# Optimization experiments

Hardware: AMD Instinct MI355X
Metric: run time of the kernel (lower is better)

## Reference

```python
import jax, jax.numpy as jnp
import numpy as np

TOPK = 4
ROUTE_SCALE = 1.0


def setup_inputs() -> dict:
    key = jax.random.key(0)
    ks = jax.random.split(key, 16)
    B, S, C, D = 4, 512, 4, 2048
    E, H = 16, 1408
    SH = 2 * H  # n_shared_experts * moe_inter_dim
    s = 0.02
    return {
        "embeddings": jax.random.normal(ks[0], (B, S, C, D), jnp.float32),
        "x": jax.random.normal(ks[1], (B, S, C, 1), jnp.float32),
        "Wg": jax.random.normal(ks[2], (E, D), jnp.float32) * s,
        "W1": jax.random.normal(ks[3], (E, H, D), jnp.float32) * s,
        "b1": jax.random.normal(ks[4], (E, H), jnp.float32) * s,
        "W2": jax.random.normal(ks[5], (E, D, H), jnp.float32) * s,
        "b2": jax.random.normal(ks[6], (E, D), jnp.float32) * s,
        "W3": jax.random.normal(ks[7], (E, H, D), jnp.float32) * s,
        "b3": jax.random.normal(ks[8], (E, H), jnp.float32) * s,
        "Ws1": jax.random.normal(ks[9], (SH, D), jnp.float32) * s,
        "bs1": jax.random.normal(ks[10], (SH,), jnp.float32) * s,
        "Ws2": jax.random.normal(ks[11], (D, SH), jnp.float32) * s,
        "bs2": jax.random.normal(ks[12], (D,), jnp.float32) * s,
    }


def reference(embeddings, x, Wg, W1, b1, W2, b2, W3, b3, Ws1, bs1, Ws2, bs2):
    # NOTE: in the torch module, the `x` arg is immediately shadowed by
    # embeddings.view(-1, dim); it does not participate in the math.
    D = Wg.shape[1]
    E = Wg.shape[0]
    xt = embeddings.reshape(-1, D)  # [N, D] flattened tokens

    # Gate: softmax scores (fp32), top-k routing; n_groups == 1, no gate bias.
    logits = jnp.einsum("nd,ed->ne", xt, Wg)
    scores = jax.nn.softmax(logits.astype(jnp.float32), axis=-1)  # [N, E]
    topv, idx = jax.lax.top_k(scores, TOPK)  # values == gathered original scores
    weights = (topv * ROUTE_SCALE).astype(xt.dtype)  # [N, K]

    # Expert dispatch/combine. Per-token combined weight for expert e is
    # sum_k weights[n, k] * (idx[n, k] == e); unassigned tokens get weight 0,
    # so masked-dense per-expert SwiGLU reproduces the gather/scatter math.
    y = jnp.zeros_like(xt)
    for e in range(E):
        w_e = jnp.sum(weights * (idx == e).astype(weights.dtype), axis=1)  # [N]
        h = jax.nn.silu(xt @ W1[e].T + b1[e]) * (xt @ W3[e].T + b3[e])  # [N, H]
        y = y + (h @ W2[e].T + b2[e]) * w_e[:, None]

    # Shared experts: Linear -> SiLU -> Linear applied to every token.
    z = jax.nn.silu(xt @ Ws1.T + bs1) @ Ws2.T + bs2

    return (y + z).reshape(embeddings.shape)
```

## Files before the change

### kernel.cpp

```cpp
#include <hip/hip_runtime.h>
#include <stdint.h>

#define N_TOK 8192
#define DIM   2048
#define NEXP  16
#define HID   1408
#define SHID  2816
#define KTOP  4
#define TILEMAX 272

typedef __attribute__((ext_vector_type(8))) short bf16x8;
typedef __attribute__((ext_vector_type(4))) float f32x4;

#define MFMA16(a,b,c) __builtin_amdgcn_mfma_f32_16x16x32_bf16((a),(b),(c),0,0,0)

__device__ __forceinline__ unsigned short f2b(float f){
  unsigned u = __float_as_uint(f);
  return (unsigned short)((u + 0x7fffu + ((u >> 16) & 1u)) >> 16);
}
__device__ __forceinline__ unsigned pk2(float a, float b){
  return (unsigned)f2b(a) | ((unsigned)f2b(b) << 16);
}
__device__ __forceinline__ float bu2f(unsigned hs){ return __uint_as_float(hs << 16); }
__device__ __forceinline__ float siluf(float x){ return x / (1.f + expf(-x)); }
__device__ __forceinline__ f32x4 zero4(){ f32x4 z; z[0]=0.f; z[1]=0.f; z[2]=0.f; z[3]=0.f; return z; }

__device__ __forceinline__ void gll16(const unsigned short* g, unsigned short* l){
  __builtin_amdgcn_global_load_lds(
      (const __attribute__((address_space(1))) void*)g,
      (__attribute__((address_space(3))) void*)l, 16, 0, 0);
}

#define SEGW ((size_t)NEXP*HID*DIM/4)
#define SEGS ((size_t)SHID*DIM/4)
__global__ __launch_bounds__(256) void k_cvtW(const float* __restrict__ W1, const float* __restrict__ W3,
                                              const float* __restrict__ W2, const float* __restrict__ Ws1,
                                              const float* __restrict__ Ws2,
                                              unsigned short* __restrict__ d1, unsigned short* __restrict__ d3,
                                              unsigned short* __restrict__ d2, unsigned short* __restrict__ ds1,
                                              unsigned short* __restrict__ ds2){
  size_t total = 3*SEGW + 2*SEGS;
  for (size_t i = (size_t)blockIdx.x*256 + threadIdx.x; i < total; i += (size_t)gridDim.x*256){
    const float* s; unsigned short* d; size_t off;
    if      (i <   SEGW)        { s = W1;  d = d1;  off = i; }
    else if (i < 2*SEGW)        { s = W3;  d = d3;  off = i - SEGW; }
    else if (i < 3*SEGW)        { s = W2;  d = d2;  off = i - 2*SEGW; }
    else if (i < 3*SEGW + SEGS) { s = Ws1; d = ds1; off = i - 3*SEGW; }
    else                        { s = Ws2; d = ds2; off = i - 3*SEGW - SEGS; }
    float4 v = ((const float4*)s)[off];
    uint2 q; q.x = pk2(v.x, v.y); q.y = pk2(v.z, v.w);
    ((uint2*)d)[off] = q;
  }
}

__global__ __launch_bounds__(256) void k_gate(const float* __restrict__ X, const float* __restrict__ Wg,
                                              float* __restrict__ topw, int* __restrict__ topi,
                                              int* __restrict__ cnt, unsigned short* __restrict__ Xb){
  int lane = threadIdx.x & 63;
  int t = blockIdx.x*4 + (threadIdx.x >> 6);
  const float* xr = X + (size_t)t*DIM;
  float4 xv[8];
#pragma unroll
  for (int i=0;i<8;i++){
    xv[i] = *(const float4*)(xr + i*256 + lane*4);
    uint2 q; q.x = pk2(xv[i].x, xv[i].y); q.y = pk2(xv[i].z, xv[i].w);
    *(uint2*)(Xb + (size_t)t*DIM + i*256 + lane*4) = q;
  }
  float sc[NEXP];
#pragma unroll
  for (int e=0;e<NEXP;e++){
    const float* wr = Wg + e*DIM;
    float s = 0.f;
#pragma unroll
    for (int i=0;i<8;i++){
      float4 w = *(const float4*)(wr + i*256 + lane*4);
      s = fmaf(xv[i].x, w.x, s); s = fmaf(xv[i].y, w.y, s);
      s = fmaf(xv[i].z, w.z, s); s = fmaf(xv[i].w, w.w, s);
    }
#pragma unroll
    for (int d=1; d<64; d<<=1) s += __shfl_xor(s, d);
    sc[e] = s;
  }
  if (lane == 0){
    float m = sc[0];
#pragma unroll
    for (int e=1;e<NEXP;e++) m = fmaxf(m, sc[e]);
    float den = 0.f;
#pragma unroll
    for (int e=0;e<NEXP;e++){ sc[e] = expf(sc[e]-m); den += sc[e]; }
    float inv = 1.f/den;
#pragma unroll
    for (int e=0;e<NEXP;e++) sc[e] *= inv;
    for (int k=0;k<KTOP;k++){
      int bi = 0; float bv = sc[0];
#pragma unroll
      for (int e=1;e<NEXP;e++) if (sc[e] > bv){ bv = sc[e]; bi = e; }
      topw[t*KTOP+k] = bv;
      topi[t*KTOP+k] = bi;
#pragma unroll
      for (int e=0;e<NEXP;e++) if (e == bi) sc[e] = -1.f;
      atomicAdd(&cnt[bi], 1);
    }
  }
}

__global__ void k_scan(const int* __restrict__ cnt, int* __restrict__ off, int* __restrict__ cur,
                       int* __restrict__ tab){
  if (threadIdx.x == 0){
    int a = 0;
    for (int e=0;e<NEXP;e++){ off[e] = a; cur[e] = a; a += cnt[e]; }
    int n = 0;
    for (int e=0;e<NEXP;e++){
      int nt = (cnt[e] + 127) >> 7;
      for (int r=0;r<nt;r++) tab[n++] = (e << 16) | r;
    }
    for (; n < TILEMAX; ++n) tab[n] = -1;
  }
}

__global__ __launch_bounds__(256) void k_place(const int* __restrict__ topi, const float* __restrict__ topw,
                                               int* __restrict__ cur, int* __restrict__ rows,
                                               float* __restrict__ rw, int* __restrict__ slotL){
  int t = blockIdx.x*256 + threadIdx.x;
#pragma unroll
  for (int k=0;k<KTOP;k++){
    int e = topi[t*KTOP+k];
    int p = atomicAdd(&cur[e], 1);
    rows[p] = t;
    rw[p]   = topw[t*KTOP+k];
    slotL[t*KTOP+k] = p;
  }
}

__device__ __forceinline__ void stage_Bf(unsigned short* lsB, const float* bF,
                                         int ldK, int bn0, int k0, int tid){
#pragma unroll
  for (int j=0;j<8;j++){
    int idx = j*256 + tid, r = idx >> 4, c4 = idx & 15;
    float4 v = *(const float4*)(bF + (size_t)(bn0 + r)*ldK + k0 + c4*4);
    uint2 q; q.x = pk2(v.x, v.y); q.y = pk2(v.z, v.w);
    *(uint2*)&lsB[r*64 + (((c4 >> 1) ^ (r & 7)) << 3) + ((c4 & 1) << 2)] = q;
  }
}

__device__ __forceinline__ void read_A(bf16x8 af[4], const unsigned short* lsA, int wm, int lane, int kc){
  int s = kc*4 + (lane >> 4);
#pragma unroll
  for (int mi=0;mi<4;mi++){
    int r = wm + mi*16 + (lane & 15);
    af[mi] = *(const bf16x8*)&lsA[r*64 + ((s ^ (r & 7)) << 3)];
  }
}

template<bool WBF>
__global__ __launch_bounds__(256,2) void k_g13(const unsigned short* __restrict__ Xb,
    const void* __restrict__ W1p, const void* __restrict__ W3p,
    const float* __restrict__ b1, const float* __restrict__ b3,
    const int* __restrict__ rows, const int* __restrict__ cnt, const int* __restrict__ offs,
    const int* __restrict__ tab, unsigned short* __restrict__ H1)
{
  int bid = blockIdx.x;
  int l = bid >> 3;
  int ct = l / 34;
  int slot = (bid & 7)*34 + (l - ct*34);
  int ent = tab[slot];
  if (ent < 0) return;
  int e = ent >> 16, rt = ent & 0xffff;
  int cntE = cnt[e];
  int offE = offs[e];
  int hn0 = ct*128;
  int tid = threadIdx.x, lane = tid & 63, wid = tid >> 6;
  int wm = (wid >> 1)*64, wn = (wid & 1)*64;
  __shared__ alignas(16) unsigned short lsA[8192], lsB1[8192], lsB3[8192];

  int lr8 = lane >> 3;
  int cx  = (lane & 7) ^ lr8;
  unsigned offA[4];
#pragma unroll
  for (int j=0;j<4;j++){
    int lrow = rt*128 + wid*32 + j*8 + lr8;
    int arow = rows[offE + (lrow < cntE ? lrow : cntE-1)];
    offA[j] = (unsigned)arow*DIM + (unsigned)cx*8;
  }
  unsigned offB0 = (unsigned)(hn0 + wid*32 + lr8)*DIM + (unsigned)cx*8;
  const unsigned short* b1H = (const unsigned short*)W1p + (size_t)e*HID*DIM;
  const unsigned short* b3H = (const unsigned short*)W3p + (size_t)e*HID*DIM;
  const float* b1F = (const float*)W1p + (size_t)e*HID*DIM;
  const float* b3F = (const float*)W3p + (size_t)e*HID*DIM;
  unsigned short* lA  = &lsA[wid*2048];
  unsigned short* lB1 = &lsB1[wid*2048];
  unsigned short* lB3 = &lsB3[wid*2048];

  f32x4 acc1[4][4], acc3[4][4];
#pragma unroll
  for (int i=0;i<4;i++)
#pragma unroll
    for (int j=0;j<4;j++){ acc1[i][j] = zero4(); acc3[i][j] = zero4(); }

  for (int kt=0; kt<DIM/64; ++kt){
    int k0 = kt*64;
    __syncthreads();
#pragma unroll
    for (int j=0;j<4;j++){
      gll16(Xb + offA[j] + k0, lA + j*512);
      if constexpr (WBF){
        gll16(b1H + offB0 + j*(8*DIM) + k0, lB1 + j*512);
        gll16(b3H + offB0 + j*(8*DIM) + k0, lB3 + j*512);
      }
    }
    if constexpr (!WBF){
      stage_Bf(lsB1, b1F, DIM, hn0, k0, tid);
      stage_Bf(lsB3, b3F, DIM, hn0, k0, tid);
    }
    __syncthreads();
#pragma unroll
    for (int kc=0;kc<2;kc++){
      bf16x8 af[4]; read_A(af, lsA, wm, lane, kc);
      int sB = kc*4 + (lane >> 4);
#pragma unroll
      for (int nj=0;nj<4;nj++){
        int rb = wn + nj*16 + (lane & 15);
        int lof = rb*64 + ((sB ^ (rb & 7)) << 3);
        bf16x8 bf1 = *(const bf16x8*)&lsB1[lof];
        bf16x8 bf3 = *(const bf16x8*)&lsB3[lof];
#pragma unroll
        for (int mi=0;mi<4;mi++){
          acc1[mi][nj] = MFMA16(af[mi], bf1, acc1[mi][nj]);
          acc3[mi][nj] = MFMA16(af[mi], bf3, acc3[mi][nj]);
        }
      }
    }
  }
#pragma unroll
  for (int nj=0;nj<4;nj++){
    int h = hn0 + wn + nj*16 + (lane & 15);
    float b1v = b1[e*HID + h];
    float b3v = b3[e*HID + h];
#pragma unroll
    for (int mi=0;mi<4;mi++){
#pragma unroll
      for (int r=0;r<4;r++){
        int gr = rt*128 + wm + mi*16 + (lane >> 4)*4 + r;
        if (gr < cntE){
          float u = acc1[mi][nj][r] + b1v;
          float v = acc3[mi][nj][r] + b3v;
          H1[(size_t)(offE + gr)*HID + h] = f2b(siluf(u)*v);
        }
      }
    }
  }
}

template<int MODE, bool WBF, int KSTEPS>
__global__ __launch_bounds__(256,2) void k_gemm(const unsigned short* __restrict__ Abase,
    const void* __restrict__ Bpv, const float* __restrict__ bias,
    float* __restrict__ outF, unsigned short* __restrict__ outH,
    const int* __restrict__ rows, const float* __restrict__ rw,
    const int* __restrict__ cnt, const int* __restrict__ offs,
    const int* __restrict__ tab)
{
  constexpr bool EXPERT = (MODE == 2 || MODE == 3);
  constexpr int KD = KSTEPS*64;
  int e = 0, ct, rt, cntE = 0, offE = 0;
  int bid = blockIdx.x;
  int l = bid >> 3;
  if constexpr (EXPERT){
    ct = l / 34;
    int slot = (bid & 7)*34 + (l - ct*34);
    int ent = tab[slot];
    if (ent < 0) return;
    e = ent >> 16; rt = ent & 0xffff;
    cntE = cnt[e];
    offE = offs[e];
  } else {
    rt = (bid & 7)*8 + (l & 7);
    ct = l >> 3;
  }
  int bn0 = ct*128, t0 = rt*128;
  int tid = threadIdx.x, lane = tid & 63, wid = tid >> 6;
  int wm = (wid >> 1)*64, wn = (wid & 1)*64;
  __shared__ alignas(16) unsigned short lsA[8192], lsB[8192];

  int lr8 = lane >> 3;
  int cx  = (lane & 7) ^ lr8;
  unsigned offA0 = 0;
  unsigned offA[4];
  if constexpr (EXPERT){
#pragma unroll
    for (int j=0;j<4;j++){
      int lrow = t0 + wid*32 + j*8 + lr8;
      int arow = offE + (lrow < cntE ? lrow : cntE-1);
      offA[j] = (unsigned)arow*KD + (unsigned)cx*8;
    }
  } else {
    offA0 = (unsigned)(t0 + wid*32 + lr8)*KD + (unsigned)cx*8;
  }
  unsigned offB0 = (unsigned)(bn0 + wid*32 + lr8)*KD + (unsigned)cx*8;
  const unsigned short* bH = (const unsigned short*)Bpv + (EXPERT ? (size_t)e*2048*KD : (size_t)0);
  const float*          bF = (const float*)Bpv          + (EXPERT ? (size_t)e*2048*KD : (size_t)0);
  const float* biasp = bias + (EXPERT ? e*DIM : 0);
  unsigned short* lA = &lsA[wid*2048];
  unsigned short* lB = &lsB[wid*2048];

  f32x4 acc[4][4];
#pragma unroll
  for (int i=0;i<4;i++)
#pragma unroll
    for (int j=0;j<4;j++) acc[i][j] = zero4();

  for (int kt=0; kt<KSTEPS; ++kt){
    int k0 = kt*64;
    __syncthreads();
#pragma unroll
    for (int j=0;j<4;j++){
      if constexpr (EXPERT) gll16(Abase + offA[j] + k0, lA + j*512);
      else                  gll16(Abase + offA0 + j*(8*KD) + k0, lA + j*512);
      if constexpr (WBF)    gll16(bH + offB0 + j*(8*KD) + k0, lB + j*512);
    }
    if constexpr (!WBF) stage_Bf(lsB, bF, KD, bn0, k0, tid);
    __syncthreads();
#pragma unroll
    for (int kc=0;kc<2;kc++){
      bf16x8 af[4]; read_A(af, lsA, wm, lane, kc);
      int sB = kc*4 + (lane >> 4);
#pragma unroll
      for (int nj=0;nj<4;nj++){
        int rb = wn + nj*16 + (lane & 15);
        bf16x8 bfr = *(const bf16x8*)&lsB[rb*64 + ((sB ^ (rb & 7)) << 3)];
#pragma unroll
        for (int mi=0;mi<4;mi++)
          acc[mi][nj] = MFMA16(af[mi], bfr, acc[mi][nj]);
      }
    }
  }
#pragma unroll
  for (int nj=0;nj<4;nj++){
    int col = bn0 + wn + nj*16 + (lane & 15);
    float bv = biasp[col];
#pragma unroll
    for (int mi=0;mi<4;mi++){
#pragma unroll
      for (int r=0;r<4;r++){
        int lr = wm + mi*16 + (lane >> 4)*4 + r;
        float v = acc[mi][nj][r] + bv;
        if constexpr (MODE == 0){
          outH[(size_t)(t0 + lr)*SHID + col] = f2b(siluf(v));
        } else if constexpr (MODE == 1){
          outF[(size_t)(t0 + lr)*DIM + col] = v;
        } else {
          int gr = t0 + lr;
          if (gr < cntE){
            int slot = offE + gr;
            float wv = rw[slot] * v;
            if constexpr (MODE == 2){
              atomicAdd(outF + (size_t)rows[slot]*DIM + col, wv);
            } else {
              outH[(size_t)slot*DIM + col] = f2b(wv);
            }
          }
        }
      }
    }
  }
}

__global__ __launch_bounds__(256) void k_comb(const unsigned short* __restrict__ Yr,
                                              const int* __restrict__ slotL, float* __restrict__ out){
  int i = blockIdx.x*256 + threadIdx.x;
  int t = i >> 8, c = i & 255;
  size_t ob = (size_t)t*DIM + (size_t)c*8;
  float4 a = *(float4*)(out + ob);
  float4 b = *(float4*)(out + ob + 4);
  int sl[4];
#pragma unroll
  for (int k=0;k<KTOP;k++) sl[k] = slotL[t*KTOP + k];
#pragma unroll
  for (int k=0;k<KTOP;k++){
    uint4 v = *(const uint4*)(Yr + (size_t)sl[k]*DIM + (size_t)c*8);
    a.x += bu2f(v.x & 0xffffu); a.y += bu2f(v.x >> 16);
    a.z += bu2f(v.y & 0xffffu); a.w += bu2f(v.y >> 16);
    b.x += bu2f(v.z & 0xffffu); b.y += bu2f(v.z >> 16);
    b.z += bu2f(v.w & 0xffffu); b.w += bu2f(v.w >> 16);
  }
  *(float4*)(out + ob) = a;
  *(float4*)(out + ob + 4) = b;
}

extern "C" void kernel_launch(void* const* d_in, const int* in_sizes, int n_in,
                              void* d_out, int out_size, void* d_ws, size_t ws_size,
                              hipStream_t stream)
{
  (void)in_sizes; (void)n_in; (void)out_size;
  const float* emb = (const float*)d_in[0];
  const float* Wg  = (const float*)d_in[2];
  const float* W1  = (const float*)d_in[3];
  const float* b1  = (const float*)d_in[4];
  const float* W2  = (const float*)d_in[5];
  const float* b2  = (const float*)d_in[6];
  const float* W3  = (const float*)d_in[7];
  const float* b3  = (const float*)d_in[8];
  const float* Ws1 = (const float*)d_in[9];
  const float* bs1 = (const float*)d_in[10];
  const float* Ws2 = (const float*)d_in[11];
  const float* bs2 = (const float*)d_in[12];
  float* out = (float*)d_out;
  char* ws = (char*)d_ws;

  const size_t SZ_XB = (size_t)N_TOK*DIM*2;
  const size_t SZ_H1 = (size_t)N_TOK*KTOP*HID*2;
  const size_t SZ_HS = (size_t)N_TOK*SHID*2;
  const size_t SZ_T4 = (size_t)N_TOK*KTOP*4;
  const size_t SZ_WB = (size_t)NEXP*HID*DIM*2;
  const size_t SZ_SB = (size_t)SHID*DIM*2;
  const size_t SZ_YR = (size_t)N_TOK*KTOP*DIM*2;

  size_t off_xb = 0;
  size_t off_h1 = off_xb + SZ_XB;
  size_t off_hs = off_h1 + SZ_H1;
  size_t off_tw = off_hs + SZ_HS;
  size_t off_ti = off_tw + SZ_T4;
  size_t off_ro = off_ti + SZ_T4;
  size_t off_rw = off_ro + SZ_T4;
  size_t off_sl = off_rw + SZ_T4;
  size_t off_cnt = off_sl + SZ_T4;
  size_t off_off = off_cnt + 256;
  size_t off_cur = off_off + 256;
  size_t off_tab = off_cur + 256;
  size_t base_end = off_tab + TILEMAX*4 + 64;
  size_t off_w1b = base_end;
  size_t off_w3b = off_w1b + SZ_WB;
  size_t off_w2b = off_w3b + SZ_WB;
  size_t off_s1b = off_w2b + SZ_WB;
  size_t off_s2b = off_s1b + SZ_SB;
  size_t wbf_end = off_s2b + SZ_SB;

  bool wbf = ws_size >= wbf_end;
  size_t off_yr = wbf ? wbf_end : base_end;
  bool comb = ws_size >= off_yr + SZ_YR;

  unsigned short* Xb = (unsigned short*)(ws + off_xb);
  unsigned short* H1 = (unsigned short*)(ws + off_h1);
  unsigned short* Hs = (unsigned short*)(ws + off_hs);
  float* topw = (float*)(ws + off_tw);
  int*   topi = (int*)(ws + off_ti);
  int*   rowsL= (int*)(ws + off_ro);
  float* rwL  = (float*)(ws + off_rw);
  int*   slotL= (int*)(ws + off_sl);
  int*   cntP = (int*)(ws + off_cnt);
  int*   offP = (int*)(ws + off_off);
  int*   curP = (int*)(ws + off_cur);
  int*   tabP = (int*)(ws + off_tab);
  unsigned short* Yr = (unsigned short*)(ws + off_yr);

  hipMemsetAsync(ws + off_cnt, 0, 768, stream);
  if (wbf){
    k_cvtW<<<4096, 256, 0, stream>>>(W1, W3, W2, Ws1, Ws2,
        (unsigned short*)(ws + off_w1b), (unsigned short*)(ws + off_w3b),
        (unsigned short*)(ws + off_w2b), (unsigned short*)(ws + off_s1b),
        (unsigned short*)(ws + off_s2b));
  }
  k_gate<<<2048, 256, 0, stream>>>(emb, Wg, topw, topi, cntP, Xb);
  k_scan<<<1, 64, 0, stream>>>(cntP, offP, curP, tabP);
  k_place<<<32, 256, 0, stream>>>(topi, topw, curP, rowsL, rwL, slotL);

  if (wbf) k_g13<true ><<<2992, 256, 0, stream>>>(Xb, ws+off_w1b, ws+off_w3b, b1, b3, rowsL, cntP, offP, tabP, H1);
  else     k_g13<false><<<2992, 256, 0, stream>>>(Xb, W1, W3, b1, b3, rowsL, cntP, offP, tabP, H1);

  if (wbf) k_gemm<0,true ,32><<<1408, 256, 0, stream>>>(Xb, ws+off_s1b, bs1, nullptr, Hs, nullptr,nullptr,nullptr,nullptr,nullptr);
  else     k_gemm<0,false,32><<<1408, 256, 0, stream>>>(Xb, Ws1, bs1, nullptr, Hs, nullptr,nullptr,nullptr,nullptr,nullptr);

  if (wbf) k_gemm<1,true ,44><<<1024, 256, 0, stream>>>(Hs, ws+off_s2b, bs2, out, nullptr, nullptr,nullptr,nullptr,nullptr,nullptr);
  else     k_gemm<1,false,44><<<1024, 256, 0, stream>>>(Hs, Ws2, bs2, out, nullptr, nullptr,nullptr,nullptr,nullptr,nullptr);

  if (comb){
    if (wbf) k_gemm<3,true ,22><<<4352, 256, 0, stream>>>(H1, ws+off_w2b, b2, nullptr, Yr, rowsL, rwL, cntP, offP, tabP);
    else     k_gemm<3,false,22><<<4352, 256, 0, stream>>>(H1, W2, b2, nullptr, Yr, rowsL, rwL, cntP, offP, tabP);
    k_comb<<<N_TOK, 256, 0, stream>>>(Yr, slotL, out);
  } else {
    if (wbf) k_gemm<2,true ,22><<<4352, 256, 0, stream>>>(H1, ws+off_w2b, b2, out, nullptr, rowsL, rwL, cntP, offP, tabP);
    else     k_gemm<2,false,22><<<4352, 256, 0, stream>>>(H1, W2, b2, out, nullptr, rowsL, rwL, cntP, offP, tabP);
  }
}
```

Baseline: 1.746 ms.

## Add 256x256-tile 512-thread bf16 GEMM for shared-down and expert-down projections

```diff
diff --git a/kernel.cpp b/kernel.cpp
--- a/kernel.cpp
+++ b/kernel.cpp
@@ -8,11 +8,18 @@
 #define SHID  2816
 #define KTOP  4
 #define TILEMAX 272
+#define TILEMAX2 144
 
 typedef __attribute__((ext_vector_type(8))) short bf16x8;
 typedef __attribute__((ext_vector_type(4))) float f32x4;
 
 #define MFMA16(a,b,c) __builtin_amdgcn_mfma_f32_16x16x32_bf16((a),(b),(c),0,0,0)
+
+#define WAIT_VM(n)  do { asm volatile("s_waitcnt vmcnt(" #n ")" ::: "memory"); \
+                         __builtin_amdgcn_sched_barrier(0); } while(0)
+#define WAIT_ALL()  do { asm volatile("s_waitcnt vmcnt(0)" ::: "memory"); \
+                         __builtin_amdgcn_sched_barrier(0); } while(0)
+#define BARRIER()   __builtin_amdgcn_s_barrier()
 
 __device__ __forceinline__ unsigned short f2b(float f){
   unsigned u = __float_as_uint(f);
@@ -105,7 +112,7 @@
 }
 
 __global__ void k_scan(const int* __restrict__ cnt, int* __restrict__ off, int* __restrict__ cur,
-                       int* __restrict__ tab){
+                       int* __restrict__ tab, int* __restrict__ tab2){
   if (threadIdx.x == 0){
     int a = 0;
     for (int e=0;e<NEXP;e++){ off[e] = a; cur[e] = a; a += cnt[e]; }
@@ -115,6 +122,12 @@
       for (int r=0;r<nt;r++) tab[n++] = (e << 16) | r;
     }
     for (; n < TILEMAX; ++n) tab[n] = -1;
+    n = 0;
+    for (int e=0;e<NEXP;e++){
+      int nt = (cnt[e] + 255) >> 8;
+      for (int r=0;r<nt;r++) tab2[n++] = (e << 16) | r;
+    }
+    for (; n < TILEMAX2; ++n) tab2[n] = -1;
   }
 }
 
@@ -364,6 +377,155 @@
   }
 }
 
+template<int MODE, int KSTEPS>
+__global__ __launch_bounds__(512,1) void k_gemm8(const unsigned short* __restrict__ Abase,
+    const unsigned short* __restrict__ Bb, const float* __restrict__ bias,
+    float* __restrict__ outF, unsigned short* __restrict__ outH,
+    const int* __restrict__ rows, const float* __restrict__ rw,
+    const int* __restrict__ cnt, const int* __restrict__ offs,
+    const int* __restrict__ tab2)
+{
+  constexpr int KD = KSTEPS*64;
+  constexpr bool EXPERT = (MODE == 3);
+  int bid = blockIdx.x, l = bid >> 3;
+  int e = 0, ct, rt, cntE = 0, offE = 0;
+  if constexpr (EXPERT){
+    ct = l / 18;
+    int slot = (bid & 7)*18 + (l - ct*18);
+    int ent = tab2[slot];
+    if (ent < 0) return;
+    e = ent >> 16; rt = ent & 0xffff;
+    cntE = cnt[e]; offE = offs[e];
+  } else {
+    rt = (bid & 7)*4 + (l & 3);
+    ct = l >> 2;
+  }
+  int bn0 = ct*256, t0 = rt*256;
+  int tid = threadIdx.x, lane = tid & 63, wid = tid >> 6;
+  int wm = (wid >> 2)*128, wn = (wid & 3)*64;
+  __shared__ alignas(16) unsigned short lsA[2][16384], lsB[2][16384];
+
+  int r0 = tid >> 3;
+  int cx = (tid & 7) ^ (r0 & 7);
+  unsigned offA[4];
+#pragma unroll
+  for (int u=0;u<4;u++){
+    int lrow = t0 + u*64 + r0;
+    int arow;
+    if constexpr (EXPERT) arow = offE + (lrow < cntE ? lrow : cntE-1);
+    else                  arow = lrow;
+    offA[u] = (unsigned)arow*KD + (unsigned)cx*8;
+  }
+  unsigned offB[4];
+#pragma unroll
+  for (int u=0;u<4;u++) offB[u] = (unsigned)(bn0 + u*64 + r0)*KD + (unsigned)cx*8;
+  const unsigned short* Bp = Bb + (EXPERT ? (size_t)e*2048*KD : (size_t)0);
+  const float* biasp = bias + (EXPERT ? e*DIM : 0);
+  unsigned dst = (unsigned)tid*8;
+
+  f32x4 acc[8][4];
+#pragma unroll
+  for (int i=0;i<8;i++)
+#pragma unroll
+    for (int j=0;j<4;j++) acc[i][j] = zero4();
+
+#define STG_A(u,b,k0)  gll16(Abase + offA[u] + (k0), &lsA[b][(u)*4096 + dst])
+#define STG_B(u,b,k0)  gll16(Bp    + offB[u] + (k0), &lsB[b][(u)*4096 + dst])
+#define RD8(ls,R,c)    (*(const bf16x8*)&(ls)[((R)>>6)*4096 + ((R)&63)*64 + ((((c)) ^ (((R)&63)&7)) << 3)])
+
+  STG_B(0,0,0); STG_B(1,0,0); STG_B(2,0,0); STG_B(3,0,0);
+  STG_A(0,0,0); STG_A(2,0,0); STG_A(1,0,0); STG_A(3,0,0);
+
+  bf16x8 bfr[2][4];
+  for (int kt=0; kt<KSTEPS; ++kt){
+    int buf = kt & 1, nb = buf ^ 1;
+    int k1 = (kt+1)*64;
+    bool pf = (kt+1 < KSTEPS);
+    WAIT_VM(2);
+    BARRIER();
+    if (pf){ STG_B(0,nb,k1); STG_B(1,nb,k1); }
+    {
+      int c0 = 0*4 + (lane >> 4);
+#pragma unroll
+      for (int nj=0;nj<4;nj++) bfr[0][nj] = RD8(lsB[buf], wn + nj*16 + (lane & 15), c0);
+      __builtin_amdgcn_s_setprio(1);
+#pragma unroll
+      for (int mi=0;mi<4;mi++){
+        bf16x8 af = RD8(lsA[buf], wm + mi*16 + (lane & 15), c0);
+#pragma unroll
+        for (int nj=0;nj<4;nj++) acc[mi][nj] = MFMA16(af, bfr[0][nj], acc[mi][nj]);
+      }
+      __builtin_amdgcn_s_setprio(0);
+    }
+    if (pf){ STG_B(2,nb,k1); STG_B(3,nb,k1); }
+    {
+      int c1 = 1*4 + (lane >> 4);
+#pragma unroll
+      for (int nj=0;nj<4;nj++) bfr[1][nj] = RD8(lsB[buf], wn + nj*16 + (lane & 15), c1);
+      __builtin_amdgcn_s_setprio(1);
+#pragma unroll
+      for (int mi=0;mi<4;mi++){
+        bf16x8 af = RD8(lsA[buf], wm + mi*16 + (lane & 15), c1);
+#pragma unroll
+        for (int nj=0;nj<4;nj++) acc[mi][nj] = MFMA16(af, bfr[1][nj], acc[mi][nj]);
+      }
+      __builtin_amdgcn_s_setprio(0);
+    }
+    if (pf) WAIT_VM(4); else WAIT_ALL();
+    BARRIER();
+    if (pf){ STG_A(0,nb,k1); STG_A(2,nb,k1); }
+    {
+      int c0 = 0*4 + (lane >> 4);
+      __builtin_amdgcn_s_setprio(1);
+#pragma unroll
+      for (int mi=4;mi<8;mi++){
+        bf16x8 af = RD8(lsA[buf], wm + mi*16 + (lane & 15), c0);
+#pragma unroll
+        for (int nj=0;nj<4;nj++) acc[mi][nj] = MFMA16(af, bfr[0][nj], acc[mi][nj]);
+      }
+      __builtin_amdgcn_s_setprio(0);
+    }
+    if (pf){ STG_A(1,nb,k1); STG_A(3,nb,k1); }
+    {
+      int c1 = 1*4 + (lane >> 4);
+      __builtin_amdgcn_s_setprio(1);
+#pragma unroll
+      for (int mi=4;mi<8;mi++){
+        bf16x8 af = RD8(lsA[buf], wm + mi*16 + (lane & 15), c1);
+#pragma unroll
+        for (int nj=0;nj<4;nj++) acc[mi][nj] = MFMA16(af, bfr[1][nj], acc[mi][nj]);
+      }
+      __builtin_amdgcn_s_setprio(0);
+    }
+  }
+#undef STG_A
+#undef STG_B
+#undef RD8
+
+#pragma unroll
+  for (int nj=0;nj<4;nj++){
+    int col = bn0 + wn + nj*16 + (lane & 15);
+    float bv = biasp[col];
+#pragma unroll
+    for (int mi=0;mi<8;mi++){
+#pragma unroll
+      for (int r=0;r<4;r++){
+        int lr = wm + mi*16 + (lane >> 4)*4 + r;
+        float v = acc[mi][nj][r] + bv;
+        if constexpr (MODE == 1){
+          outF[(size_t)(t0 + lr)*DIM + col] = v;
+        } else {
+          int gr = t0 + lr;
+          if (gr < cntE){
+            int slot = offE + gr;
+            outH[(size_t)slot*DIM + col] = f2b(rw[slot] * v);
+          }
+        }
+      }
+    }
+  }
+}
+
 __global__ __launch_bounds__(256) void k_comb(const unsigned short* __restrict__ Yr,
                                               const int* __restrict__ slotL, float* __restrict__ out){
   int i = blockIdx.x*256 + threadIdx.x;
@@ -426,7 +588,8 @@
   size_t off_off = off_cnt + 256;
   size_t off_cur = off_off + 256;
   size_t off_tab = off_cur + 256;
-  size_t base_end = off_tab + TILEMAX*4 + 64;
+  size_t off_tab2 = off_tab + TILEMAX*4;
+  size_t base_end = off_tab2 + TILEMAX2*4 + 64;
   size_t off_w1b = base_end;
   size_t off_w3b = off_w1b + SZ_WB;
   size_t off_w2b = off_w3b + SZ_WB;
@@ -450,6 +613,7 @@
   int*   offP = (int*)(ws + off_off);
   int*   curP = (int*)(ws + off_cur);
   int*   tabP = (int*)(ws + off_tab);
+  int*   tab2P= (int*)(ws + off_tab2);
   unsigned short* Yr = (unsigned short*)(ws + off_yr);
 
   hipMemsetAsync(ws + off_cnt, 0, 768, stream);
@@ -460,7 +624,7 @@
         (unsigned short*)(ws + off_s2b));
   }
   k_gate<<<2048, 256, 0, stream>>>(emb, Wg, topw, topi, cntP, Xb);
-  k_scan<<<1, 64, 0, stream>>>(cntP, offP, curP, tabP);
+  k_scan<<<1, 64, 0, stream>>>(cntP, offP, curP, tabP, tab2P);
   k_place<<<32, 256, 0, stream>>>(topi, topw, curP, rowsL, rwL, slotL);
 
   if (wbf) k_g13<true ><<<2992, 256, 0, stream>>>(Xb, ws+off_w1b, ws+off_w3b, b1, b3, rowsL, cntP, offP, tabP, H1);
@@ -469,14 +633,19 @@
   if (wbf) k_gemm<0,true ,32><<<1408, 256, 0, stream>>>(Xb, ws+off_s1b, bs1, nullptr, Hs, nullptr,nullptr,nullptr,nullptr,nullptr);
   else     k_gemm<0,false,32><<<1408, 256, 0, stream>>>(Xb, Ws1, bs1, nullptr, Hs, nullptr,nullptr,nullptr,nullptr,nullptr);
 
-  if (wbf) k_gemm<1,true ,44><<<1024, 256, 0, stream>>>(Hs, ws+off_s2b, bs2, out, nullptr, nullptr,nullptr,nullptr,nullptr,nullptr);
-  else     k_gemm<1,false,44><<<1024, 256, 0, stream>>>(Hs, Ws2, bs2, out, nullptr, nullptr,nullptr,nullptr,nullptr,nullptr);
-
-  if (comb){
-    if (wbf) k_gemm<3,true ,22><<<4352, 256, 0, stream>>>(H1, ws+off_w2b, b2, nullptr, Yr, rowsL, rwL, cntP, offP, tabP);
-    else     k_gemm<3,false,22><<<4352, 256, 0, stream>>>(H1, W2, b2, nullptr, Yr, rowsL, rwL, cntP, offP, tabP);
+  if (wbf && comb){
+    k_gemm8<1,44><<<256, 512, 0, stream>>>(Hs, (unsigned short*)(ws+off_s2b), bs2, out, nullptr,
+                                           nullptr, nullptr, nullptr, nullptr, nullptr);
+    k_gemm8<3,22><<<1152, 512, 0, stream>>>(H1, (unsigned short*)(ws+off_w2b), b2, nullptr, Yr,
+                                            rowsL, rwL, cntP, offP, tab2P);
+    k_comb<<<N_TOK, 256, 0, stream>>>(Yr, slotL, out);
+  } else if (comb){
+    k_gemm<1,false,44><<<1024, 256, 0, stream>>>(Hs, Ws2, bs2, out, nullptr, nullptr,nullptr,nullptr,nullptr,nullptr);
+    k_gemm<3,false,22><<<4352, 256, 0, stream>>>(H1, W2, b2, nullptr, Yr, rowsL, rwL, cntP, offP, tabP);
     k_comb<<<N_TOK, 256, 0, stream>>>(Yr, slotL, out);
   } else {
+    if (wbf) k_gemm<1,true ,44><<<1024, 256, 0, stream>>>(Hs, ws+off_s2b, bs2, out, nullptr, nullptr,nullptr,nullptr,nullptr,nullptr);
+    else     k_gemm<1,false,44><<<1024, 256, 0, stream>>>(Hs, Ws2, bs2, out, nullptr, nullptr,nullptr,nullptr,nullptr,nullptr);
     if (wbf) k_gemm<2,true ,22><<<4352, 256, 0, stream>>>(H1, ws+off_w2b, b2, out, nullptr, rowsL, rwL, cntP, offP, tabP);
     else     k_gemm<2,false,22><<<4352, 256, 0, stream>>>(H1, W2, b2, out, nullptr, rowsL, rwL, cntP, offP, tabP);
   }
```

Result: slower. 2.035 ms (+16.5%).
